# Optimization experiments

Hardware: AMD Instinct MI355X
Metric: run time of the kernel (lower is better)

The kernel has to match this reference:

```python
import jax, jax.numpy as jnp
import numpy as np

DIM = 2048
H = 16
HD = DIM // H          # 128
ROPE_CH = (HD // 2) // 2 * 2  # 64
EPS = 1e-6
SCALE = HD ** -0.5
MAX_WAVELENGTH = 10000.0


def rmsnorm(v, w):
    vf = v.astype(jnp.float32)
    var = jnp.mean(vf * vf, axis=-1, keepdims=True)
    return (w * (vf * jax.lax.rsqrt(var + EPS))).astype(v.dtype)


def apply_rope(v, pos):
    # v: [B, S, H, C], pos: [B, S]
    C = v.shape[-1]
    frac = 2.0 * jnp.arange(C // 2, dtype=jnp.float32) / C
    timescale = MAX_WAVELENGTH ** frac                      # [C/2]
    ang = pos[:, :, None].astype(jnp.float32) / timescale   # [B, S, C/2]
    ang = ang[:, :, None, :]                                 # [B, S, 1, C/2]
    sin, cos = jnp.sin(ang), jnp.cos(ang)
    v1, v2 = jnp.split(v, 2, axis=-1)
    return jnp.concatenate([v1 * cos - v2 * sin, v2 * cos + v1 * sin], axis=-1).astype(v.dtype)


def apply_rotary_emb(v, pos, channels):
    # rope only the last `channels` of head_dim
    left, right = v[..., :-channels], v[..., -channels:]
    return jnp.concatenate([left, apply_rope(right, pos)], axis=-1)


def project_qkv(t, W, b, qn, kn):
    B, N, _ = t.shape
    qkv = t @ W + b                                          # [B, N, 3*H*HD]
    q, k, v = jnp.split(qkv, [H * HD, 2 * H * HD], axis=-1)
    q = rmsnorm(q.reshape(B, N, H, HD), qn)
    k = rmsnorm(k.reshape(B, N, H, HD), kn)
    v = v.reshape(B, N, H, HD)
    return q, k, v


def setup_inputs() -> dict:
    key = jax.random.key(0)
    ks = jax.random.split(key, 12)
    B, NX, NY = 2, 2048, 512
    x = jax.random.normal(ks[0], (B, NX, DIM), dtype=jnp.float32)
    y = jax.random.normal(ks[1], (B, NY, DIM), dtype=jnp.float32)
    temporal_pos = jax.random.randint(ks[2], (B, NX), 0, 2048)
    y_temporal_pos = jax.random.randint(ks[3], (B, NY), 0, 512)
    s = 0.02
    Wqkv_x = jax.random.normal(ks[4], (DIM, 3 * H * HD), dtype=jnp.float32) * s
    bqkv_x = jnp.zeros((3 * H * HD,), dtype=jnp.float32)
    Wqkv_y = jax.random.normal(ks[5], (DIM, 3 * H * HD), dtype=jnp.float32) * s
    bqkv_y = jnp.zeros((3 * H * HD,), dtype=jnp.float32)
    Wproj_x = jax.random.normal(ks[6], (DIM, DIM), dtype=jnp.float32) * s
    bproj_x = jnp.zeros((DIM,), dtype=jnp.float32)
    Wproj_y = jax.random.normal(ks[7], (DIM, DIM), dtype=jnp.float32) * s
    bproj_y = jnp.zeros((DIM,), dtype=jnp.float32)
    qnx = jnp.ones((HD,), dtype=jnp.float32)
    knx = jnp.ones((HD,), dtype=jnp.float32)
    qny = jnp.ones((HD,), dtype=jnp.float32)
    kny = jnp.ones((HD,), dtype=jnp.float32)
    return {"x": x, "y": y, "temporal_pos": temporal_pos, "y_temporal_pos": y_temporal_pos,
            "Wqkv_x": Wqkv_x, "bqkv_x": bqkv_x, "qnx": qnx, "knx": knx,
            "Wproj_x": Wproj_x, "bproj_x": bproj_x,
            "Wqkv_y": Wqkv_y, "bqkv_y": bqkv_y, "qny": qny, "kny": kny,
            "Wproj_y": Wproj_y, "bproj_y": bproj_y}


def reference(x, y, temporal_pos, y_temporal_pos,
              Wqkv_x, bqkv_x, qnx, knx, Wproj_x, bproj_x,
              Wqkv_y, bqkv_y, qny, kny, Wproj_y, bproj_y):
    B, NX, _ = x.shape
    NY = y.shape[1]
    qx, kx, vx = project_qkv(x, Wqkv_x, bqkv_x, qnx, knx)   # [B, NX, H, HD]
    qy, ky, vy = project_qkv(y, Wqkv_y, bqkv_y, qny, kny)   # [B, NY, H, HD]
    # RoPE on last ROPE_CH channels of head_dim (rope_dim=-1)
    qx = apply_rotary_emb(qx, temporal_pos, ROPE_CH)
    kx = apply_rotary_emb(kx, temporal_pos, ROPE_CH)
    qy = apply_rotary_emb(qy, y_temporal_pos, ROPE_CH)
    ky = apply_rotary_emb(ky, y_temporal_pos, ROPE_CH)
    # joint attention over concatenated x/y tokens
    q = jnp.concatenate([qx, qy], axis=1)   # [B, S, H, HD]
    k = jnp.concatenate([kx, ky], axis=1)
    v = jnp.concatenate([vx, vy], axis=1)
    scores = jnp.einsum('bqhd,bkhd->bhqk', q, k) * SCALE
    attn = jax.nn.softmax(scores, axis=-1)
    out = jnp.einsum('bhqk,bkhd->bqhd', attn, v)             # [B, S, H, HD]
    out = out.reshape(B, NX + NY, DIM).astype(x.dtype)
    x_out = out[:, :NX] @ Wproj_x + bproj_x
    y_out = out[:, NX:] @ Wproj_y + bproj_y
    return (x_out, y_out)
```

## Files before the change

kernel.cpp:

```cpp
#include <hip/hip_runtime.h>
#include <stdint.h>

typedef __attribute__((ext_vector_type(8))) short v8s;
typedef __attribute__((ext_vector_type(4))) float v4f;

#define DEV static __device__ __forceinline__

DEV unsigned short f2bf(float f) {
  union { float f; unsigned int u; } v; v.f = f;
  unsigned int u = v.u;
  return (unsigned short)((u + 0x7fffu + ((u >> 16) & 1u)) >> 16);
}

DEV v4f mfma16(v8s a, v8s b, v4f c) {
  return __builtin_amdgcn_mfma_f32_16x16x32_bf16(a, b, c, 0, 0, 0);
}

DEV unsigned int cvtpk(float lo, float hi) {
  unsigned int r;
  asm("v_cvt_pk_bf16_f32 %0, %1, %2" : "=v"(r) : "v"(lo), "v"(hi));
  return r;
}

DEV float aexp2(float x) {
  float r;
  asm("v_exp_f32 %0, %1" : "=v"(r) : "v"(x));
  return r;
}

DEV void async16(const void* g, void* lds) {
  __builtin_amdgcn_global_load_lds((const __attribute__((address_space(1))) unsigned int*)g,
                                   (__attribute__((address_space(3))) unsigned int*)lds,
                                   16, 0, 0);
}

__global__ __launch_bounds__(256) void k_f32_to_bf16(const float* __restrict__ in,
                                                     unsigned short* __restrict__ out, int n4) {
  int i = blockIdx.x * 256 + threadIdx.x;
  if (i < n4) {
    float4 v = reinterpret_cast<const float4*>(in)[i];
    ushort4 o;
    o.x = f2bf(v.x); o.y = f2bf(v.y); o.z = f2bf(v.z); o.w = f2bf(v.w);
    reinterpret_cast<ushort4*>(out)[i] = o;
  }
}

__global__ __launch_bounds__(256) void k_rope_tbl(const int* __restrict__ pos,
                                                  float* __restrict__ tbl, int nrows) {
  int idx = blockIdx.x * 256 + threadIdx.x;
  if (idx < nrows * 32) {
    int row = idx >> 5, i = idx & 31;
    float ang = (float)pos[row] * expf((float)i * -0.2878231366f);
    float sv, cv;
    sincosf(ang, &sv, &cv);
    reinterpret_cast<float2*>(tbl)[(size_t)row * 32 + i] = make_float2(cv, sv);
  }
}

__global__ __launch_bounds__(256) void k_transpose(const float* __restrict__ in,
                                                   unsigned short* __restrict__ out, int R, int C) {
  __shared__ float tile[64][65];
  const int r0 = blockIdx.x * 64, c0 = blockIdx.y * 64;
  const int t = threadIdx.x;
  const int rl = t >> 4, cl = (t & 15) * 4;
#pragma unroll
  for (int p = 0; p < 4; p++) {
    const int r = rl + p * 16;
    float4 v = *reinterpret_cast<const float4*>(&in[(size_t)(r0 + r) * C + c0 + cl]);
    tile[r][cl] = v.x; tile[r][cl + 1] = v.y; tile[r][cl + 2] = v.z; tile[r][cl + 3] = v.w;
  }
  __syncthreads();
  const int cw = t >> 4, rw = (t & 15) * 4;
#pragma unroll
  for (int p = 0; p < 4; p++) {
    const int c = cw + p * 16;
    ushort4 o;
    o.x = f2bf(tile[rw + 0][c]); o.y = f2bf(tile[rw + 1][c]);
    o.z = f2bf(tile[rw + 2][c]); o.w = f2bf(tile[rw + 3][c]);
    *reinterpret_cast<ushort4*>(&out[(size_t)(c0 + c) * R + r0 + rw]) = o;
  }
}

template <int MODE>
__global__ __launch_bounds__(512, 4) void k_gemm(
    const unsigned short* __restrict__ A, const unsigned short* __restrict__ Bt,
    const float* __restrict__ bias, float* __restrict__ Cout,
    unsigned short* __restrict__ Qb, unsigned short* __restrict__ Kb,
    unsigned short* __restrict__ Vt, const float* __restrict__ qn,
    const float* __restrict__ kn, const float* __restrict__ rtbl, int K, int N, int Nm, int noff,
    int rows_per_b, int b_stride, int row_off, int Mb) {
  __shared__ __align__(16) char Lds[3 * 24576];
  const int chunk = gridDim.x >> 3;
  const int o = (blockIdx.x & 7) * chunk + (blockIdx.x >> 3);
  const int m0 = (o % Mb) * 128, n0 = (o / Mb) * 256;
  const int t = threadIdx.x, l = t & 63, w = t >> 6;
  const int lg = l >> 4, li = l & 15;
  const int wr = w >> 1, wc = w & 1;

  auto amap = [&](int m) -> size_t {
    return (size_t)(m / rows_per_b) * b_stride + row_off + (m % rows_per_b);
  };
  const int ar = t >> 2, as = t & 3;
  const int asw = (as ^ ((ar >> 1) & 3)) * 8;
  const unsigned short* ap = A + amap(m0 + ar) * K + asw;
  const unsigned short* bp0 = Bt + (size_t)(n0 + ar) * K + asw;
  const unsigned short* bp1 = bp0 + (size_t)128 * K;
  const int t16 = t * 16;

  auto stage = [&](char* lb, int st) {
    const int ko = st * 32;
    async16(ap + ko, lb + t16);
    async16(bp0 + ko, lb + 8192 + t16);
    async16(bp1 + ko, lb + 16384 + t16);
  };

  int aoff[2], boff[8];
#pragma unroll
  for (int mf = 0; mf < 2; mf++) {
    const int row = wr * 32 + mf * 16 + li;
    aoff[mf] = row * 64 + ((lg ^ ((row >> 1) & 3)) * 16);
  }
#pragma unroll
  for (int nf = 0; nf < 8; nf++) {
    const int row = wc * 128 + nf * 16 + li;
    boff[nf] = 8192 + row * 64 + ((lg ^ ((row >> 1) & 3)) * 16);
  }

  v4f acc[2][8] = {};
  const int NK = K >> 5;

  stage(Lds, 0);
  stage(Lds + 24576, 1);

  int bufc = 0;
  for (int tt = 0; tt < NK; tt++) {
    asm volatile("s_waitcnt vmcnt(3)" ::: "memory");
    __builtin_amdgcn_sched_barrier(0);
    __builtin_amdgcn_s_barrier();
    __builtin_amdgcn_sched_barrier(0);
    int nb = bufc + 49152;
    if (nb >= 73728) nb -= 73728;
    stage(Lds + nb, (tt + 2 < NK) ? tt + 2 : NK - 1);
    char* Bf = Lds + bufc;
    v8s af0 = *reinterpret_cast<const v8s*>(Bf + aoff[0]);
    v8s af1 = *reinterpret_cast<const v8s*>(Bf + aoff[1]);
    __builtin_amdgcn_s_setprio(1);
#pragma unroll
    for (int nf = 0; nf < 8; nf++) {
      v8s bfv = *reinterpret_cast<const v8s*>(Bf + boff[nf]);
      acc[0][nf] = mfma16(af0, bfv, acc[0][nf]);
      acc[1][nf] = mfma16(af1, bfv, acc[1][nf]);
    }
    __builtin_amdgcn_s_setprio(0);
    bufc += 24576;
    if (bufc == 73728) bufc = 0;
  }
  asm volatile("s_waitcnt vmcnt(0)" ::: "memory");

#pragma unroll
  for (int nf = 0; nf < 8; nf++) {
    const float bv = bias[n0 + wc * 128 + nf * 16 + li];
#pragma unroll
    for (int mf = 0; mf < 2; mf++)
#pragma unroll
      for (int r = 0; r < 4; r++) acc[mf][nf][r] += bv;
  }

  if (MODE == 0) {
#pragma unroll
    for (int mf = 0; mf < 2; mf++) {
      const int row = m0 + wr * 32 + mf * 16 + lg * 4;
#pragma unroll
      for (int nf = 0; nf < 8; nf++) {
        const int col = n0 + wc * 128 + nf * 16 + li;
#pragma unroll
        for (int r = 0; r < 4; r++) Cout[(size_t)(row + r) * N + col] = acc[mf][nf][r];
      }
    }
    return;
  }

  const int sec = n0 >> 11;
  const int hh = ((n0 + wc * 128) >> 7) & 15;
  const int mrow0 = m0 + wr * 32;

  if (sec < 2) {
    const float* gw = (sec == 0) ? qn : kn;
    unsigned short* Out = (sec == 0) ? Qb : Kb;
    float g[8];
#pragma unroll
    for (int nf = 0; nf < 8; nf++) g[nf] = gw[nf * 16 + li];
#pragma unroll
    for (int mf = 0; mf < 2; mf++) {
#pragma unroll
      for (int r = 0; r < 4; r++) {
        float s = 0.f;
#pragma unroll
        for (int nf = 0; nf < 8; nf++) s += acc[mf][nf][r] * acc[mf][nf][r];
#pragma unroll
        for (int off = 1; off < 16; off <<= 1) s += __shfl_xor(s, off, 64);
        const int m = mrow0 + mf * 16 + lg * 4 + r;
        const float rn = rsqrtf(s * (1.0f / 128.0f) + 1e-6f);
        float vv[8];
#pragma unroll
        for (int nf = 0; nf < 8; nf++) vv[nf] = acc[mf][nf][r] * rn * g[nf];
#pragma unroll
        for (int nf = 4; nf < 6; nf++) {
          const float2 cs =
              reinterpret_cast<const float2*>(rtbl)[(size_t)m * 32 + (nf - 4) * 16 + li];
          const float v1 = vv[nf], v2 = vv[nf + 2];
          vv[nf] = v1 * cs.x - v2 * cs.y;
          vv[nf + 2] = v2 * cs.x + v1 * cs.y;
        }
        const int b = m / Nm, n = m - b * Nm;
        const size_t base = ((size_t)(b * 16 + hh) * 2560 + noff + n) * 128;
#pragma unroll
        for (int nf = 0; nf < 8; nf++) Out[base + nf * 16 + li] = f2bf(vv[nf]);
      }
    }
  } else {
#pragma unroll
    for (int mf = 0; mf < 2; mf++) {
      const int m = mrow0 + mf * 16 + lg * 4;
      const int b = m / Nm, n = m - b * Nm;
      const int key = noff + n;
      const size_t base = ((size_t)(b * 16 + hh) * 80 + (key >> 5)) * 4096 + (key & 31);
#pragma unroll
      for (int nf = 0; nf < 8; nf++) {
        const int chan = nf * 16 + li;
        ushort4 ov;
        ov.x = f2bf(acc[mf][nf][0]); ov.y = f2bf(acc[mf][nf][1]);
        ov.z = f2bf(acc[mf][nf][2]); ov.w = f2bf(acc[mf][nf][3]);
        *reinterpret_cast<ushort4*>(&Vt[base + chan * 32]) = ov;
      }
    }
  }
}

__global__ __launch_bounds__(256) void k_attn(const unsigned short* __restrict__ Qb,
                                              const unsigned short* __restrict__ Kb,
                                              const unsigned short* __restrict__ Vt,
                                              unsigned short* __restrict__ Ob) {
  __shared__ __align__(16) char Ldss[3 * 16384];
  const int NT = 2560;
  const float SC2 = 0.12751744737492888f;
  const float FM2 = 17.312340490667560f;
  const int i = blockIdx.x;
  const int xcd = i & 7, j = i >> 3;
  const int qt = j % 20;
  const int bh = xcd * 4 + j / 20;
  const int b = bh >> 4, h = bh & 15;
  const int t = threadIdx.x, l = t & 63, w = t >> 6;
  const int lg = l >> 4, li = l & 15;
  const unsigned short* Qbase = Qb + ((size_t)bh * NT + qt * 128) * 128;
  const unsigned short* Kbase = Kb + (size_t)bh * NT * 128;
  const unsigned short* Vbase = Vt + (size_t)bh * 327680;

  v8s qf[2][4];
#pragma unroll
  for (int mg = 0; mg < 2; mg++) {
    const int row = w * 32 + mg * 16 + li;
#pragma unroll
    for (int ds = 0; ds < 4; ds++)
      qf[mg][ds] = *reinterpret_cast<const v8s*>(Qbase + (size_t)row * 128 + (lg + ds * 4) * 8);
  }

  const char* kg[2];
  const char* vg[2];
  int kd[2], vd[2];
#pragma unroll
  for (int p = 0; p < 2; p++) {
    const int rho = w * 4 + (l >> 4) + p * 16;
    const int key = ((rho >> 2) & 3) * 8 + ((rho >> 4) & 1) * 4 + (rho & 3);
    kg[p] = (const char*)Kbase + (size_t)key * 256 + (((l & 15) ^ (rho & 7)) * 16);
    kd[p] = w * 1024 + p * 4096;
    const int d = w * 32 + p * 16 + (l >> 2);
    vg[p] = (const char*)Vbase + (size_t)d * 64 + ((((l & 3) * 2) ^ (d & 6)) * 8);
    vd[p] = 8192 + w * 2048 + p * 1024;
  }
  auto stage = [&](char* lb, int st) {
    const size_t so = (size_t)st * 8192;
    async16(kg[0] + so, lb + kd[0]);
    async16(kg[1] + so, lb + kd[1]);
    async16(vg[0] + so, lb + vd[0]);
    async16(vg[1] + so, lb + vd[1]);
  };

  int koff[2][4], voff[8];
#pragma unroll
  for (int kf = 0; kf < 2; kf++)
#pragma unroll
    for (int ds = 0; ds < 4; ds++) {
      const int row = kf * 16 + li;
      koff[kf][ds] = row * 256 + (((lg + ds * 4) ^ (row & 7)) * 16);
    }
#pragma unroll
  for (int df = 0; df < 8; df++) {
    const int d = df * 16 + li;
    voff[df] = 8192 + d * 64 + (((lg * 2) ^ (d & 6)) * 8);
  }

  float ps[2] = {0.f, 0.f};
  v4f O_[2][8] = {};

  stage(Ldss, 0);
  stage(Ldss + 16384, 1);

  int bufc = 0;
  for (int tt = 0; tt < 80; tt++) {
    asm volatile("s_waitcnt vmcnt(4)" ::: "memory");
    __builtin_amdgcn_sched_barrier(0);
    __builtin_amdgcn_s_barrier();
    __builtin_amdgcn_sched_barrier(0);
    int nb = bufc + 32768;
    if (nb >= 49152) nb -= 49152;
    stage(Ldss + nb, (tt + 2 < 80) ? tt + 2 : 79);
    char* B = Ldss + bufc;

    v4f s[2][2] = {};
    __builtin_amdgcn_s_setprio(1);
#pragma unroll
    for (int kf = 0; kf < 2; kf++)
#pragma unroll
      for (int ds = 0; ds < 4; ds++) {
        v8s ka = *reinterpret_cast<const v8s*>(B + koff[kf][ds]);
        s[0][kf] = mfma16(ka, qf[0][ds], s[0][kf]);
        s[1][kf] = mfma16(ka, qf[1][ds], s[1][kf]);
      }
    __builtin_amdgcn_s_setprio(0);

    v8s pa[2];
#pragma unroll
    for (int mg = 0; mg < 2; mg++) {
      float p[2][4];
#pragma unroll
      for (int kf = 0; kf < 2; kf++)
#pragma unroll
        for (int r = 0; r < 4; r++)
          p[kf][r] = aexp2(fmaf(s[mg][kf][r], SC2, -FM2));
      const float t0 = (p[0][0] + p[0][1]) + (p[0][2] + p[0][3]);
      const float t1 = (p[1][0] + p[1][1]) + (p[1][2] + p[1][3]);
      ps[mg] += t0 + t1;
      union { v8s v; unsigned int u[4]; } pk;
      pk.u[0] = cvtpk(p[0][0], p[0][1]);
      pk.u[1] = cvtpk(p[0][2], p[0][3]);
      pk.u[2] = cvtpk(p[1][0], p[1][1]);
      pk.u[3] = cvtpk(p[1][2], p[1][3]);
      pa[mg] = pk.v;
    }

    __builtin_amdgcn_s_setprio(1);
#pragma unroll
    for (int df = 0; df < 8; df++) {
      v8s vb = *reinterpret_cast<const v8s*>(B + voff[df]);
      O_[0][df] = mfma16(pa[0], vb, O_[0][df]);
      O_[1][df] = mfma16(pa[1], vb, O_[1][df]);
    }
    __builtin_amdgcn_s_setprio(0);

    bufc += 16384;
    if (bufc == 49152) bufc = 0;
  }
  asm volatile("s_waitcnt vmcnt(0)" ::: "memory");

#pragma unroll
  for (int mg = 0; mg < 2; mg++) {
    ps[mg] += __shfl_xor(ps[mg], 16, 64);
    ps[mg] += __shfl_xor(ps[mg], 32, 64);
  }
#pragma unroll
  for (int mg = 0; mg < 2; mg++) {
    float inv[4];
#pragma unroll
    for (int r = 0; r < 4; r++) inv[r] = 1.0f / __shfl(ps[mg], lg * 4 + r, 64);
#pragma unroll
    for (int df = 0; df < 8; df++) {
      const int d = df * 16 + li;
#pragma unroll
      for (int r = 0; r < 4; r++) {
        const int q = qt * 128 + w * 32 + mg * 16 + lg * 4 + r;
        Ob[((size_t)b * NT + q) * 2048 + h * 128 + d] = f2bf(O_[mg][df][r] * inv[r]);
      }
    }
  }
}

extern "C" void kernel_launch(void* const* d_in, const int* in_sizes, int n_in,
                              void* d_out, int out_size, void* d_ws, size_t ws_size,
                              hipStream_t stream) {
  (void)in_sizes; (void)n_in; (void)out_size;
  const float* x = (const float*)d_in[0];
  const float* y = (const float*)d_in[1];
  const int* tpos = (const int*)d_in[2];
  const int* ypos = (const int*)d_in[3];
  const float* Wqkv_x = (const float*)d_in[4];
  const float* bqkv_x = (const float*)d_in[5];
  const float* qnx = (const float*)d_in[6];
  const float* knx = (const float*)d_in[7];
  const float* Wproj_x = (const float*)d_in[8];
  const float* bproj_x = (const float*)d_in[9];
  const float* Wqkv_y = (const float*)d_in[10];
  const float* bqkv_y = (const float*)d_in[11];
  const float* qny = (const float*)d_in[12];
  const float* kny = (const float*)d_in[13];
  const float* Wproj_y = (const float*)d_in[14];
  const float* bproj_y = (const float*)d_in[15];
  float* outp = (float*)d_out;

  char* ws = (char*)d_ws;
  size_t off = 0;
  auto alloc = [&](size_t b) {
    char* p = ws + off;
    off += (b + 255) & ~(size_t)255;
    return p;
  };
  unsigned short* Wt = (unsigned short*)alloc(6144ull * 2048 * 2);
  unsigned short* xb = (unsigned short*)alloc(4096ull * 2048 * 2);
  unsigned short* yb = (unsigned short*)alloc(1024ull * 2048 * 2);
  unsigned short* Qbf = (unsigned short*)alloc(2ull * 16 * 2560 * 128 * 2);
  unsigned short* Kbf = (unsigned short*)alloc(2ull * 16 * 2560 * 128 * 2);
  unsigned short* Vtb = (unsigned short*)alloc(2ull * 16 * 80 * 128 * 32 * 2);
  unsigned short* Obf = (unsigned short*)alloc(2ull * 2560 * 2048 * 2);
  float* rtx = (float*)alloc(4096ull * 64 * 4);
  float* rty = (float*)alloc(1024ull * 64 * 4);
  if (ws_size < off) return;

  k_f32_to_bf16<<<8192, 256, 0, stream>>>(x, xb, 2097152);
  k_f32_to_bf16<<<2048, 256, 0, stream>>>(y, yb, 524288);
  k_rope_tbl<<<512, 256, 0, stream>>>(tpos, rtx, 4096);
  k_rope_tbl<<<128, 256, 0, stream>>>(ypos, rty, 1024);

  k_transpose<<<dim3(32, 96), 256, 0, stream>>>(Wqkv_x, Wt, 2048, 6144);
  k_gemm<1><<<768, 512, 0, stream>>>(xb, Wt, bqkv_x, nullptr, Qbf, Kbf, Vtb, qnx, knx, rtx, 2048,
                                     6144, 2048, 0, 4096, 0, 0, 32);
  k_transpose<<<dim3(32, 96), 256, 0, stream>>>(Wqkv_y, Wt, 2048, 6144);
  k_gemm<1><<<192, 512, 0, stream>>>(yb, Wt, bqkv_y, nullptr, Qbf, Kbf, Vtb, qny, kny, rty, 2048,
                                     6144, 512, 2048, 1024, 0, 0, 8);

  k_attn<<<640, 256, 0, stream>>>(Qbf, Kbf, Vtb, Obf);

  k_transpose<<<dim3(32, 32), 256, 0, stream>>>(Wproj_x, Wt, 2048, 2048);
  k_gemm<0><<<256, 512, 0, stream>>>(Obf, Wt, bproj_x, outp, nullptr, nullptr, nullptr, nullptr,
                                     nullptr, nullptr, 2048, 2048, 0, 0, 2048, 2560, 0, 32);
  k_transpose<<<dim3(32, 32), 256, 0, stream>>>(Wproj_y, Wt, 2048, 2048);
  k_gemm<0><<<64, 512, 0, stream>>>(Obf, Wt, bproj_y, outp + 8388608ull, nullptr, nullptr, nullptr,
                                    nullptr, nullptr, nullptr, 2048, 2048, 0, 0, 512, 2560, 2048,
                                    8);
}
```

Baseline: 428.8 us.

## Halve attention query tile and load V fragments directly from global memory

The attention kernel now handles 64 queries per block instead of 128, launching twice as many blocks with a launch-bounds hint for four blocks per CU. Only K is staged through LDS; V fragments are read straight from global memory into registers each iteration, which shrinks shared memory to 24KB. The aim is higher occupancy and less LDS traffic. In exchange, K and V are reloaded twice as often across blocks and V global-load latency now sits on the critical path before the PV MFMAs.

After: 535.9 us. 1.25x slower.

```diff
diff --git a/kernel.cpp b/kernel.cpp
--- a/kernel.cpp
+++ b/kernel.cpp
@@ -237,56 +237,49 @@
   }
 }
 
-__global__ __launch_bounds__(256) void k_attn(const unsigned short* __restrict__ Qb,
-                                              const unsigned short* __restrict__ Kb,
-                                              const unsigned short* __restrict__ Vt,
-                                              unsigned short* __restrict__ Ob) {
-  __shared__ __align__(16) char Ldss[3 * 16384];
+__global__ __launch_bounds__(256, 4) void k_attn(const unsigned short* __restrict__ Qb,
+                                                 const unsigned short* __restrict__ Kb,
+                                                 const unsigned short* __restrict__ Vt,
+                                                 unsigned short* __restrict__ Ob) {
+  __shared__ __align__(16) char Ldss[3 * 8192];
   const int NT = 2560;
   const float SC2 = 0.12751744737492888f;
   const float FM2 = 17.312340490667560f;
   const int i = blockIdx.x;
   const int xcd = i & 7, j = i >> 3;
-  const int qt = j % 20;
-  const int bh = xcd * 4 + j / 20;
+  const int qt = j % 40;
+  const int bh = xcd * 4 + j / 40;
   const int b = bh >> 4, h = bh & 15;
   const int t = threadIdx.x, l = t & 63, w = t >> 6;
   const int lg = l >> 4, li = l & 15;
-  const unsigned short* Qbase = Qb + ((size_t)bh * NT + qt * 128) * 128;
+  const unsigned short* Qbase = Qb + ((size_t)bh * NT + qt * 64) * 128;
   const unsigned short* Kbase = Kb + (size_t)bh * NT * 128;
-  const unsigned short* Vbase = Vt + (size_t)bh * 327680;
-
-  v8s qf[2][4];
-#pragma unroll
-  for (int mg = 0; mg < 2; mg++) {
-    const int row = w * 32 + mg * 16 + li;
+  const char* Vg = (const char*)(Vt + (size_t)bh * 327680);
+
+  v8s qf[4];
+  {
+    const unsigned short* qrow = Qbase + (size_t)(w * 16 + li) * 128;
 #pragma unroll
     for (int ds = 0; ds < 4; ds++)
-      qf[mg][ds] = *reinterpret_cast<const v8s*>(Qbase + (size_t)row * 128 + (lg + ds * 4) * 8);
+      qf[ds] = *reinterpret_cast<const v8s*>(qrow + (lg + ds * 4) * 8);
   }
 
   const char* kg[2];
-  const char* vg[2];
-  int kd[2], vd[2];
+  int kd[2];
 #pragma unroll
   for (int p = 0; p < 2; p++) {
-    const int rho = w * 4 + (l >> 4) + p * 16;
+    const int rho = (t >> 4) + p * 16;
     const int key = ((rho >> 2) & 3) * 8 + ((rho >> 4) & 1) * 4 + (rho & 3);
-    kg[p] = (const char*)Kbase + (size_t)key * 256 + (((l & 15) ^ (rho & 7)) * 16);
-    kd[p] = w * 1024 + p * 4096;
-    const int d = w * 32 + p * 16 + (l >> 2);
-    vg[p] = (const char*)Vbase + (size_t)d * 64 + ((((l & 3) * 2) ^ (d & 6)) * 8);
-    vd[p] = 8192 + w * 2048 + p * 1024;
+    kg[p] = (const char*)Kbase + (size_t)key * 256 + (((t & 15) ^ (rho & 7)) * 16);
+    kd[p] = t * 16 + p * 4096;
   }
   auto stage = [&](char* lb, int st) {
     const size_t so = (size_t)st * 8192;
     async16(kg[0] + so, lb + kd[0]);
     async16(kg[1] + so, lb + kd[1]);
-    async16(vg[0] + so, lb + vd[0]);
-    async16(vg[1] + so, lb + vd[1]);
   };
 
-  int koff[2][4], voff[8];
+  int koff[2][4];
 #pragma unroll
   for (int kf = 0; kf < 2; kf++)
 #pragma unroll
@@ -294,93 +287,76 @@
       const int row = kf * 16 + li;
       koff[kf][ds] = row * 256 + (((lg + ds * 4) ^ (row & 7)) * 16);
     }
+  const int vlane = li * 64 + lg * 16;
+
+  float ps = 0.f;
+  v4f O_[8] = {};
+
+  stage(Ldss, 0);
+  stage(Ldss + 8192, 1);
+  asm volatile("s_waitcnt vmcnt(2)" ::: "memory");
+
+  int bufc = 0;
+  for (int tt = 0; tt < 80; tt++) {
+    __builtin_amdgcn_s_barrier();
+    __builtin_amdgcn_sched_barrier(0);
+
+    const char* vt = Vg + (size_t)tt * 8192 + vlane;
+    v8s vb[8];
+#pragma unroll
+    for (int df = 0; df < 8; df++)
+      vb[df] = *reinterpret_cast<const v8s*>(vt + df * 1024);
+
+    int nb = bufc + 16384;
+    if (nb >= 24576) nb -= 24576;
+    stage(Ldss + nb, (tt + 2 < 80) ? tt + 2 : 79);
+
+    v4f s[2] = {};
+    __builtin_amdgcn_s_setprio(1);
+#pragma unroll
+    for (int kf = 0; kf < 2; kf++)
+#pragma unroll
+      for (int ds = 0; ds < 4; ds++) {
+        v8s ka = *reinterpret_cast<const v8s*>(Ldss + bufc + koff[kf][ds]);
+        s[kf] = mfma16(ka, qf[ds], s[kf]);
+      }
+    __builtin_amdgcn_s_setprio(0);
+
+    float p[2][4];
+#pragma unroll
+    for (int kf = 0; kf < 2; kf++)
+#pragma unroll
+      for (int r = 0; r < 4; r++) p[kf][r] = aexp2(fmaf(s[kf][r], SC2, -FM2));
+    ps += ((p[0][0] + p[0][1]) + (p[0][2] + p[0][3])) +
+          ((p[1][0] + p[1][1]) + (p[1][2] + p[1][3]));
+    union { v8s v; unsigned int u[4]; } pk;
+    pk.u[0] = cvtpk(p[0][0], p[0][1]);
+    pk.u[1] = cvtpk(p[0][2], p[0][3]);
+    pk.u[2] = cvtpk(p[1][0], p[1][1]);
+    pk.u[3] = cvtpk(p[1][2], p[1][3]);
+
+    __builtin_amdgcn_s_setprio(1);
+#pragma unroll
+    for (int df = 0; df < 8; df++) O_[df] = mfma16(pk.v, vb[df], O_[df]);
+    __builtin_amdgcn_s_setprio(0);
+
+    bufc += 8192;
+    if (bufc == 24576) bufc = 0;
+  }
+  asm volatile("s_waitcnt vmcnt(0)" ::: "memory");
+
+  ps += __shfl_xor(ps, 16, 64);
+  ps += __shfl_xor(ps, 32, 64);
+  float inv[4];
+#pragma unroll
+  for (int r = 0; r < 4; r++) inv[r] = 1.0f / __shfl(ps, lg * 4 + r, 64);
 #pragma unroll
   for (int df = 0; df < 8; df++) {
     const int d = df * 16 + li;
-    voff[df] = 8192 + d * 64 + (((lg * 2) ^ (d & 6)) * 8);
-  }
-
-  float ps[2] = {0.f, 0.f};
-  v4f O_[2][8] = {};
-
-  stage(Ldss, 0);
-  stage(Ldss + 16384, 1);
-
-  int bufc = 0;
-  for (int tt = 0; tt < 80; tt++) {
-    asm volatile("s_waitcnt vmcnt(4)" ::: "memory");
-    __builtin_amdgcn_sched_barrier(0);
-    __builtin_amdgcn_s_barrier();
-    __builtin_amdgcn_sched_barrier(0);
-    int nb = bufc + 32768;
-    if (nb >= 49152) nb -= 49152;
-    stage(Ldss + nb, (tt + 2 < 80) ? tt + 2 : 79);
-    char* B = Ldss + bufc;
-
-    v4f s[2][2] = {};
-    __builtin_amdgcn_s_setprio(1);
-#pragma unroll
-    for (int kf = 0; kf < 2; kf++)
-#pragma unroll
-      for (int ds = 0; ds < 4; ds++) {
-        v8s ka = *reinterpret_cast<const v8s*>(B + koff[kf][ds]);
-        s[0][kf] = mfma16(ka, qf[0][ds], s[0][kf]);
-        s[1][kf] = mfma16(ka, qf[1][ds], s[1][kf]);
-      }
-    __builtin_amdgcn_s_setprio(0);
-
-    v8s pa[2];
-#pragma unroll
-    for (int mg = 0; mg < 2; mg++) {
-      float p[2][4];
-#pragma unroll
-      for (int kf = 0; kf < 2; kf++)
-#pragma unroll
-        for (int r = 0; r < 4; r++)
-          p[kf][r] = aexp2(fmaf(s[mg][kf][r], SC2, -FM2));
-      const float t0 = (p[0][0] + p[0][1]) + (p[0][2] + p[0][3]);
-      const float t1 = (p[1][0] + p[1][1]) + (p[1][2] + p[1][3]);
-      ps[mg] += t0 + t1;
-      union { v8s v; unsigned int u[4]; } pk;
-      pk.u[0] = cvtpk(p[0][0], p[0][1]);
-      pk.u[1] = cvtpk(p[0][2], p[0][3]);
-      pk.u[2] = cvtpk(p[1][0], p[1][1]);
-      pk.u[3] = cvtpk(p[1][2], p[1][3]);
-      pa[mg] = pk.v;
-    }
-
-    __builtin_amdgcn_s_setprio(1);
-#pragma unroll
-    for (int df = 0; df < 8; df++) {
-      v8s vb = *reinterpret_cast<const v8s*>(B + voff[df]);
-      O_[0][df] = mfma16(pa[0], vb, O_[0][df]);
-      O_[1][df] = mfma16(pa[1], vb, O_[1][df]);
-    }
-    __builtin_amdgcn_s_setprio(0);
-
-    bufc += 16384;
-    if (bufc == 49152) bufc = 0;
-  }
-  asm volatile("s_waitcnt vmcnt(0)" ::: "memory");
-
-#pragma unroll
-  for (int mg = 0; mg < 2; mg++) {
-    ps[mg] += __shfl_xor(ps[mg], 16, 64);
-    ps[mg] += __shfl_xor(ps[mg], 32, 64);
-  }
-#pragma unroll
-  for (int mg = 0; mg < 2; mg++) {
-    float inv[4];
-#pragma unroll
-    for (int r = 0; r < 4; r++) inv[r] = 1.0f / __shfl(ps[mg], lg * 4 + r, 64);
-#pragma unroll
-    for (int df = 0; df < 8; df++) {
-      const int d = df * 16 + li;
-#pragma unroll
-      for (int r = 0; r < 4; r++) {
-        const int q = qt * 128 + w * 32 + mg * 16 + lg * 4 + r;
-        Ob[((size_t)b * NT + q) * 2048 + h * 128 + d] = f2bf(O_[mg][df][r] * inv[r]);
-      }
+#pragma unroll
+    for (int r = 0; r < 4; r++) {
+      const int q = qt * 64 + w * 16 + lg * 4 + r;
+      Ob[((size_t)b * NT + q) * 2048 + h * 128 + d] = f2bf(O_[df][r] * inv[r]);
     }
   }
 }
@@ -437,7 +413,7 @@
   k_gemm<1><<<192, 512, 0, stream>>>(yb, Wt, bqkv_y, nullptr, Qbf, Kbf, Vtb, qny, kny, rty, 2048,
                                      6144, 512, 2048, 1024, 0, 0, 8);
 
-  k_attn<<<640, 256, 0, stream>>>(Qbf, Kbf, Vtb, Obf);
+  k_attn<<<1280, 256, 0, stream>>>(Qbf, Kbf, Vtb, Obf);
 
   k_transpose<<<dim3(32, 32), 256, 0, stream>>>(Wproj_x, Wt, 2048, 2048);
   k_gemm<0><<<256, 512, 0, stream>>>(Obf, Wt, bproj_x, outp, nullptr, nullptr, nullptr, nullptr,
```
